# Performance work log

Hardware: AMD Instinct MI355X
Metric: run time of the kernel (lower is better)

The kernel has to match this reference:

```python
import jax, jax.numpy as jnp
import numpy as np

N_NODES = 50000
N_EDGES = 800000
IN_CH = 256
HID = 512
NUM_LAYERS = 3
EPS = 1e-12  # F.normalize eps


def setup_inputs() -> dict:
    key = jax.random.key(0)
    ks = jax.random.split(key, 2 + 3 * NUM_LAYERS)
    x = jax.random.normal(ks[0], (N_NODES, IN_CH), dtype=jnp.float32)
    edge_index = jax.random.randint(ks[1], (2, N_EDGES), 0, N_NODES, dtype=jnp.int64)
    inp = {"x": x, "edge_index": edge_index}
    dims = [(IN_CH, HID)] + [(HID, HID)] * (NUM_LAYERS - 1)
    for i, (din, dout) in enumerate(dims):
        s = 1.0 / np.sqrt(din)
        inp[f"Wl{i}"] = jax.random.normal(ks[2 + 3 * i], (din, dout), dtype=jnp.float32) * s
        inp[f"bl{i}"] = jnp.zeros((dout,), dtype=jnp.float32)
        inp[f"Wr{i}"] = jax.random.normal(ks[3 + 3 * i], (din, dout), dtype=jnp.float32) * s
    return inp


def _sage_conv(x, src, dst, Wl, bl, Wr):
    # aggr='add': out[dst] += x[src], then lin_l(agg) + lin_r(x), L2 normalize rows
    agg = jax.ops.segment_sum(x[src], dst, num_segments=x.shape[0])  # [N, din]
    out = agg @ Wl + bl + x @ Wr  # [N, dout]
    norm = jnp.maximum(jnp.linalg.norm(out, axis=-1, keepdims=True), EPS)
    return out / norm


def reference(x, edge_index, Wl0, bl0, Wr0, Wl1, bl1, Wr1, Wl2, bl2, Wr2):
    src, dst = edge_index[0], edge_index[1]
    feat = x
    params = [(Wl0, bl0, Wr0), (Wl1, bl1, Wr1), (Wl2, bl2, Wr2)]
    for Wl, bl, Wr in params:
        aggre = _sage_conv(feat, src, dst, Wl, bl, Wr)
        # Dropout(p=0.15) is identity in eval mode
        feat = jax.nn.elu(aggre)
    return feat
```

## Files before the change

### kernel.cpp

```cpp
#include <hip/hip_runtime.h>
#include <math.h>

#define N_NODES 50000
#define M_PAD   50048
#define N_EDGES 800000
#define HID 512

typedef short bf16x8 __attribute__((ext_vector_type(8)));
typedef float f32x4  __attribute__((ext_vector_type(4)));
typedef unsigned short u16x8 __attribute__((ext_vector_type(8)));

__device__ inline float b2f(unsigned short u) {
    union { unsigned int i; float f; } v; v.i = ((unsigned int)u) << 16; return v.f;
}
__device__ inline unsigned short f2b(float f) {
    union { float f; unsigned int i; } v; v.f = f;
    unsigned int r = v.i + 0x7FFFu + ((v.i >> 16) & 1u);
    return (unsigned short)(r >> 16);
}


__global__ void zero_kernel(int* __restrict__ p, int n) {
    int i = blockIdx.x * blockDim.x + threadIdx.x;
    if (i < n) p[i] = 0;
}

__global__ void detect_kernel(const int* __restrict__ e, int* __restrict__ flag) {
    if (blockIdx.x == 0 && threadIdx.x == 0) {
        int is64 = 1;
        for (int i = 0; i < 16; ++i)
            if (e[2 * i + 1] != 0) is64 = 0;
        *flag = is64;
    }
}

__global__ void hist_kernel(const void* __restrict__ eidx, const int* __restrict__ flag,
                            int* __restrict__ counts) {
    int e = blockIdx.x * blockDim.x + threadIdx.x;
    if (e >= N_EDGES) return;
    int is64 = *flag;
    int d;
    if (is64) d = (int)((const long long*)eidx)[N_EDGES + e];
    else      d = ((const int*)eidx)[N_EDGES + e];
    atomicAdd(&counts[d], 1);
}

__global__ __launch_bounds__(1024) void scan_kernel(const int* __restrict__ counts,
                                                    int* __restrict__ offsets) {
    __shared__ int sums[1024];
    int t = threadIdx.x;
    const int CH = (N_NODES + 1023) / 1024;
    int lo = t * CH;
    int hi = min(lo + CH, N_NODES);
    int s = 0;
    for (int i = lo; i < hi; ++i) s += counts[i];
    sums[t] = s;
    __syncthreads();
    for (int off = 1; off < 1024; off <<= 1) {
        int v = 0;
        if (t >= off) v = sums[t - off];
        __syncthreads();
        sums[t] += v;
        __syncthreads();
    }
    int excl = (t == 0) ? 0 : sums[t - 1];
    for (int i = lo; i < hi; ++i) { offsets[i] = excl; excl += counts[i]; }
    if (t == 1023) offsets[N_NODES] = excl;
}

__global__ void fill_kernel(const void* __restrict__ eidx, const int* __restrict__ flag,
                            const int* __restrict__ offsets, int* __restrict__ cursor,
                            int* __restrict__ edge_src) {
    int e = blockIdx.x * blockDim.x + threadIdx.x;
    if (e >= N_EDGES) return;
    int is64 = *flag;
    int s, d;
    if (is64) {
        const long long* p = (const long long*)eidx;
        s = (int)p[e];
        d = (int)p[N_EDGES + e];
    } else {
        const int* p = (const int*)eidx;
        s = p[e];
        d = p[N_EDGES + e];
    }
    int pos = atomicAdd(&cursor[d], 1);
    edge_src[offsets[d] + pos] = s;
}


__global__ __launch_bounds__(256) void xconv_kernel(const float* __restrict__ x,
                                                    unsigned short* __restrict__ cat1) {
    int id = blockIdx.x * 256 + threadIdx.x;
    if (id >= M_PAD * 64) return;
    int row = id >> 6;
    int c = (id & 63) * 4;
    float4 v = make_float4(0.f, 0.f, 0.f, 0.f);
    if (row < N_NODES) v = *(const float4*)(x + (size_t)row * 256 + c);
    ushort4 h;
    h.x = f2b(v.x); h.y = f2b(v.y); h.z = f2b(v.z); h.w = f2b(v.w);
    *(ushort4*)(cat1 + (size_t)row * 512 + 256 + c) = h;
}

__global__ __launch_bounds__(128) void wconv_kernel(const float* __restrict__ W,
                                                    unsigned short* __restrict__ T,
                                                    int K, int ktot, int off) {
    int n = blockIdx.x;
    for (int k = threadIdx.x; k < K; k += 128)
        T[(size_t)n * ktot + off + k] = f2b(W[(size_t)k * HID + n]);
}


template <int W>
__global__ __launch_bounds__(256) void aggregate_kernel(const unsigned short* __restrict__ Fh,
                                                        const int* __restrict__ off,
                                                        const int* __restrict__ esrc,
                                                        unsigned short* __restrict__ Ah) {
    const int NSLICE = W / 64;
    const int STRIDE = 2 * W;
    const int slice = blockIdx.x % NSLICE;
    const int chunk = blockIdx.x / NSLICE;
    const int wid = threadIdx.x >> 6;
    const int lane = threadIdx.x & 63;
    const int node = chunk * 4 + wid;
    if (node >= N_NODES) return;
    const int beg = off[node], end = off[node + 1];
    const int deg = end - beg;
    const int col = slice * 64 + lane;

    float a0 = 0.f, a1 = 0.f, a2 = 0.f, a3 = 0.f;
    int idxv = 0;
    int i = 0;
    for (; i + 4 <= deg; i += 4) {
        const int b = i & 63;
        if (b == 0) idxv = (beg + i + lane < end) ? esrc[beg + i + lane] : 0;
        const int s0 = __shfl(idxv, b);
        const int s1 = __shfl(idxv, b + 1);
        const int s2 = __shfl(idxv, b + 2);
        const int s3 = __shfl(idxv, b + 3);
        a0 += b2f(Fh[(size_t)s0 * STRIDE + col]);
        a1 += b2f(Fh[(size_t)s1 * STRIDE + col]);
        a2 += b2f(Fh[(size_t)s2 * STRIDE + col]);
        a3 += b2f(Fh[(size_t)s3 * STRIDE + col]);
    }
    for (; i < deg; ++i) {
        const int b = i & 63;
        if (b == 0) idxv = (beg + i + lane < end) ? esrc[beg + i + lane] : 0;
        a0 += b2f(Fh[(size_t)__shfl(idxv, b) * STRIDE + col]);
    }
    Ah[(size_t)node * STRIDE + col] = f2b(a0 + a1 + a2 + a3);
}


template <int FINAL>
__global__ __launch_bounds__(512, 2) void gemm_mfma_kernel(
    const unsigned short* __restrict__ A, const unsigned short* __restrict__ B,
    const float* __restrict__ bias, float* __restrict__ outF,
    unsigned short* __restrict__ pre, int K) {
    __shared__ unsigned short S[2 * 12288];
    const int bm = blockIdx.y * 128;
    const int bn = blockIdx.x * 256;
    const int tid = threadIdx.x;
    const int l = tid & 63;
    const int w = tid >> 6;
    const int wr = (w >> 2) * 64;
    const int wc = (w & 3) * 64;

    const int se = (tid >> 2) * 32 + (tid & 3) * 8;
    const unsigned short* gA  = A + (size_t)(bm + (tid >> 2)) * K + (tid & 3) * 8;
    const unsigned short* gB0 = B + (size_t)(bn + (tid >> 2)) * K + (tid & 3) * 8;
    const unsigned short* gB1 = B + (size_t)(bn + 128 + (tid >> 2)) * K + (tid & 3) * 8;

    f32x4 acc[4][4];
#pragma unroll
    for (int m = 0; m < 4; ++m)
#pragma unroll
        for (int n = 0; n < 4; ++n) acc[m][n] = (f32x4){0.f, 0.f, 0.f, 0.f};

    const int aoff = (wr + (l & 15)) * 32 + (l >> 4) * 8;
    const int woff = 4096 + (wc + (l & 15)) * 32 + (l >> 4) * 8;
    const int ktiles = K >> 5;

    auto STAGE = [&](int buf, int kt) {
        unsigned short* lb = &S[buf * 12288];
        __builtin_amdgcn_global_load_lds(
            (const __attribute__((address_space(1))) void*)(gA + kt * 32),
            (__attribute__((address_space(3))) void*)(lb + se), 16, 0, 0);
        __builtin_amdgcn_global_load_lds(
            (const __attribute__((address_space(1))) void*)(gB0 + kt * 32),
            (__attribute__((address_space(3))) void*)(lb + 4096 + se), 16, 0, 0);
        __builtin_amdgcn_global_load_lds(
            (const __attribute__((address_space(1))) void*)(gB1 + kt * 32),
            (__attribute__((address_space(3))) void*)(lb + 8192 + se), 16, 0, 0);
    };

    STAGE(0, 0);
    __syncthreads();

    for (int kt = 0; kt < ktiles; ++kt) {
        if (kt + 1 < ktiles) STAGE((kt + 1) & 1, kt + 1);
        const int sb = (kt & 1) * 12288;

        bf16x8 af[4], wf[4];
#pragma unroll
        for (int m = 0; m < 4; ++m)
            af[m] = *(const bf16x8*)&S[sb + aoff + m * 512];
#pragma unroll
        for (int n = 0; n < 4; ++n)
            wf[n] = *(const bf16x8*)&S[sb + woff + n * 512];
#pragma unroll
        for (int m = 0; m < 4; ++m)
#pragma unroll
            for (int n = 0; n < 4; ++n)
                acc[m][n] = __builtin_amdgcn_mfma_f32_16x16x32_bf16(af[m], wf[n], acc[m][n], 0, 0, 0);
        __syncthreads();
    }

    const int r0 = bm + wr + (l >> 4) * 4;
    const int c0 = bn + wc + (l & 15);
#pragma unroll
    for (int n = 0; n < 4; ++n) {
        const float bv = bias[c0 + n * 16];
#pragma unroll
        for (int m = 0; m < 4; ++m) {
#pragma unroll
            for (int j = 0; j < 4; ++j) {
                int gr = r0 + m * 16 + j;
                if (gr < N_NODES) {
                    float val = acc[m][n][j] + bv;
                    if constexpr (FINAL)
                        outF[(size_t)gr * HID + c0 + n * 16] = val;
                    else
                        pre[(size_t)gr * HID + c0 + n * 16] = f2b(val);
                }
            }
        }
    }
}


template <int FINAL>
__global__ __launch_bounds__(256) void norm_elu_kernel(const void* __restrict__ inp,
                                                       float* __restrict__ outF,
                                                       unsigned short* __restrict__ Fh) {
    const int wid = threadIdx.x >> 6;
    const int lane = threadIdx.x & 63;
    const int row = blockIdx.x * 4 + wid;
    if (row >= N_NODES) return;
    float r[8];
    if constexpr (FINAL) {
        const float* p = (const float*)inp + (size_t)row * HID + lane * 8;
        float4 v0 = *(const float4*)p;
        float4 v1 = *(const float4*)(p + 4);
        r[0] = v0.x; r[1] = v0.y; r[2] = v0.z; r[3] = v0.w;
        r[4] = v1.x; r[5] = v1.y; r[6] = v1.z; r[7] = v1.w;
    } else {
        const unsigned short* p = (const unsigned short*)inp + (size_t)row * HID + lane * 8;
        u16x8 v = *(const u16x8*)p;
#pragma unroll
        for (int j = 0; j < 8; ++j) r[j] = b2f(v[j]);
    }
    float ss = 0.f;
#pragma unroll
    for (int j = 0; j < 8; ++j) ss += r[j] * r[j];
#pragma unroll
    for (int o = 32; o > 0; o >>= 1) ss += __shfl_xor(ss, o);
    float inv = 1.f / fmaxf(sqrtf(ss), 1e-12f);
#pragma unroll
    for (int j = 0; j < 8; ++j) {
        r[j] *= inv;
        r[j] = r[j] > 0.f ? r[j] : expm1f(r[j]);
    }
    if constexpr (FINAL) {
        float* q = outF + (size_t)row * HID + lane * 8;
        *(float4*)q = make_float4(r[0], r[1], r[2], r[3]);
        *(float4*)(q + 4) = make_float4(r[4], r[5], r[6], r[7]);
    } else {
        unsigned short* q = Fh + (size_t)row * 1024 + lane * 8;
        u16x8 h;
#pragma unroll
        for (int j = 0; j < 8; ++j) h[j] = f2b(r[j]);
        *(u16x8*)q = h;
    }
}


extern "C" void kernel_launch(void* const* d_in, const int* in_sizes, int n_in,
                              void* d_out, int out_size, void* d_ws, size_t ws_size,
                              hipStream_t stream) {
    const float* x    = (const float*)d_in[0];
    const void*  eidx = d_in[1];
    const float* Wl0 = (const float*)d_in[2];
    const float* bl0 = (const float*)d_in[3];
    const float* Wr0 = (const float*)d_in[4];
    const float* Wl1 = (const float*)d_in[5];
    const float* bl1 = (const float*)d_in[6];
    const float* Wr1 = (const float*)d_in[7];
    const float* Wl2 = (const float*)d_in[8];
    const float* bl2 = (const float*)d_in[9];
    const float* Wr2 = (const float*)d_in[10];
    float* outF = (float*)d_out;
    unsigned short* preB = (unsigned short*)d_out;

    char* ws = (char*)d_ws;
    size_t o = 0;
    auto alloc = [&](size_t bytes) { void* p = ws + o; o += (bytes + 255) & ~(size_t)255; return p; };

    unsigned short* Cat1 = (unsigned short*)alloc((size_t)M_PAD * 512 * 2);
    unsigned short* Cat2 = (unsigned short*)alloc((size_t)M_PAD * 1024 * 2);

    unsigned short* Wcat0 = (unsigned short*)alloc(512 * 512 * 2);
    unsigned short* Wcat1 = (unsigned short*)alloc(512 * 1024 * 2);
    unsigned short* Wcat2 = (unsigned short*)alloc(512 * 1024 * 2);

    int* counts   = (int*)alloc((size_t)2 * N_NODES * 4);
    int* cursor   = counts + N_NODES;
    int* offsets  = (int*)alloc((size_t)(N_NODES + 1) * 4);
    int* edge_src = (int*)alloc((size_t)N_EDGES * 4);
    int* flag     = (int*)alloc(256);

    zero_kernel<<<(2 * N_NODES + 255) / 256, 256, 0, stream>>>(counts, 2 * N_NODES);
    detect_kernel<<<1, 64, 0, stream>>>((const int*)eidx, flag);
    hist_kernel<<<(N_EDGES + 255) / 256, 256, 0, stream>>>(eidx, flag, counts);
    scan_kernel<<<1, 1024, 0, stream>>>(counts, offsets);
    fill_kernel<<<(N_EDGES + 255) / 256, 256, 0, stream>>>(eidx, flag, offsets, cursor, edge_src);

    xconv_kernel<<<(M_PAD * 64 + 255) / 256, 256, 0, stream>>>(x, Cat1);
    wconv_kernel<<<512, 128, 0, stream>>>(Wl0, Wcat0, 256, 512, 0);
    wconv_kernel<<<512, 128, 0, stream>>>(Wr0, Wcat0, 256, 512, 256);
    wconv_kernel<<<512, 128, 0, stream>>>(Wl1, Wcat1, 512, 1024, 0);
    wconv_kernel<<<512, 128, 0, stream>>>(Wr1, Wcat1, 512, 1024, 512);
    wconv_kernel<<<512, 128, 0, stream>>>(Wl2, Wcat2, 512, 1024, 0);
    wconv_kernel<<<512, 128, 0, stream>>>(Wr2, Wcat2, 512, 1024, 512);

    dim3 ggrid(2, M_PAD / 128);
    const int nchunk = (N_NODES + 3) / 4;

    aggregate_kernel<256><<<nchunk * 4, 256, 0, stream>>>(Cat1 + 256, offsets, edge_src, Cat1);
    gemm_mfma_kernel<0><<<ggrid, 512, 0, stream>>>(Cat1, Wcat0, bl0, nullptr, preB, 512);
    norm_elu_kernel<0><<<nchunk, 256, 0, stream>>>(preB, nullptr, Cat2 + 512);

    aggregate_kernel<512><<<nchunk * 8, 256, 0, stream>>>(Cat2 + 512, offsets, edge_src, Cat2);
    gemm_mfma_kernel<0><<<ggrid, 512, 0, stream>>>(Cat2, Wcat1, bl1, nullptr, preB, 1024);
    norm_elu_kernel<0><<<nchunk, 256, 0, stream>>>(preB, nullptr, Cat2 + 512);

    aggregate_kernel<512><<<nchunk * 8, 256, 0, stream>>>(Cat2 + 512, offsets, edge_src, Cat2);
    gemm_mfma_kernel<1><<<ggrid, 512, 0, stream>>>(Cat2, Wcat2, bl2, outF, nullptr, 1024);
    norm_elu_kernel<1><<<nchunk, 256, 0, stream>>>(outF, outF, nullptr);

    (void)in_sizes; (void)n_in; (void)out_size; (void)ws_size;
}
```

Baseline: 919.1 us.

## Widen aggregate gathers to bf16 pairs and remap GEMM blocks per XCD

The aggregation kernel now has each lane load two adjacent bf16 values as one 32-bit word. Each wave therefore covers 128 columns, and the grid is halved, which cuts load instructions and improves gather efficiency for the latency-bound edge aggregation. The GEMM launches as a 1D grid and remaps block ids so that consecutive tiles land on the same XCD, aiming to improve L2 reuse of A rows across the two N tiles. Each loop iteration now unrolls 2 edges instead of 4, so fewer loads are in flight per iteration.

```diff
diff --git a/kernel.cpp b/kernel.cpp
--- a/kernel.cpp
+++ b/kernel.cpp
@@ -17,6 +17,12 @@
     union { float f; unsigned int i; } v; v.f = f;
     unsigned int r = v.i + 0x7FFFu + ((v.i >> 16) & 1u);
     return (unsigned short)(r >> 16);
+}
+__device__ inline float blo(unsigned int d) {
+    union { unsigned int i; float f; } v; v.i = d << 16; return v.f;
+}
+__device__ inline float bhi(unsigned int d) {
+    union { unsigned int i; float f; } v; v.i = d & 0xFFFF0000u; return v.f;
 }
 
 
@@ -116,7 +122,7 @@
                                                         const int* __restrict__ off,
                                                         const int* __restrict__ esrc,
                                                         unsigned short* __restrict__ Ah) {
-    const int NSLICE = W / 64;
+    const int NSLICE = W / 128;
     const int STRIDE = 2 * W;
     const int slice = blockIdx.x % NSLICE;
     const int chunk = blockIdx.x / NSLICE;
@@ -126,29 +132,31 @@
     if (node >= N_NODES) return;
     const int beg = off[node], end = off[node + 1];
     const int deg = end - beg;
-    const int col = slice * 64 + lane;
+    const int col = slice * 128 + lane * 2;
+    const unsigned short* F = Fh + col;
 
     float a0 = 0.f, a1 = 0.f, a2 = 0.f, a3 = 0.f;
     int idxv = 0;
     int i = 0;
-    for (; i + 4 <= deg; i += 4) {
+    for (; i + 2 <= deg; i += 2) {
         const int b = i & 63;
         if (b == 0) idxv = (beg + i + lane < end) ? esrc[beg + i + lane] : 0;
         const int s0 = __shfl(idxv, b);
         const int s1 = __shfl(idxv, b + 1);
-        const int s2 = __shfl(idxv, b + 2);
-        const int s3 = __shfl(idxv, b + 3);
-        a0 += b2f(Fh[(size_t)s0 * STRIDE + col]);
-        a1 += b2f(Fh[(size_t)s1 * STRIDE + col]);
-        a2 += b2f(Fh[(size_t)s2 * STRIDE + col]);
-        a3 += b2f(Fh[(size_t)s3 * STRIDE + col]);
-    }
-    for (; i < deg; ++i) {
+        const unsigned int v0 = *(const unsigned int*)(F + (size_t)s0 * STRIDE);
+        const unsigned int v1 = *(const unsigned int*)(F + (size_t)s1 * STRIDE);
+        a0 += blo(v0); a1 += bhi(v0);
+        a2 += blo(v1); a3 += bhi(v1);
+    }
+    if (i < deg) {
         const int b = i & 63;
         if (b == 0) idxv = (beg + i + lane < end) ? esrc[beg + i + lane] : 0;
-        a0 += b2f(Fh[(size_t)__shfl(idxv, b) * STRIDE + col]);
-    }
-    Ah[(size_t)node * STRIDE + col] = f2b(a0 + a1 + a2 + a3);
+        const unsigned int v0 = *(const unsigned int*)(F + (size_t)__shfl(idxv, b) * STRIDE);
+        a0 += blo(v0); a1 += bhi(v0);
+    }
+    const unsigned int outd =
+        (unsigned int)f2b(a0 + a2) | ((unsigned int)f2b(a1 + a3) << 16);
+    *(unsigned int*)(Ah + (size_t)node * STRIDE + col) = outd;
 }
 
 
@@ -158,8 +166,14 @@
     const float* __restrict__ bias, float* __restrict__ outF,
     unsigned short* __restrict__ pre, int K) {
     __shared__ unsigned short S[2 * 12288];
-    const int bm = blockIdx.y * 128;
-    const int bn = blockIdx.x * 256;
+    const int T = gridDim.x;
+    const int q = T >> 3, r = T & 7;
+    const int xcd = blockIdx.x & 7;
+    const int n0 = blockIdx.x >> 3;
+    const int g = xcd * q + min(xcd, r) + n0;
+    const int bm = (g >> 1) * 128;
+    const int bn = (g & 1) * 256;
+
     const int tid = threadIdx.x;
     const int l = tid & 63;
     const int w = tid >> 6;
@@ -175,7 +189,7 @@
 #pragma unroll
     for (int m = 0; m < 4; ++m)
 #pragma unroll
-        for (int n = 0; n < 4; ++n) acc[m][n] = (f32x4){0.f, 0.f, 0.f, 0.f};
+        for (int nn = 0; nn < 4; ++nn) acc[m][nn] = (f32x4){0.f, 0.f, 0.f, 0.f};
 
     const int aoff = (wr + (l & 15)) * 32 + (l >> 4) * 8;
     const int woff = 4096 + (wc + (l & 15)) * 32 + (l >> 4) * 8;
@@ -206,32 +220,32 @@
         for (int m = 0; m < 4; ++m)
             af[m] = *(const bf16x8*)&S[sb + aoff + m * 512];
 #pragma unroll
-        for (int n = 0; n < 4; ++n)
-            wf[n] = *(const bf16x8*)&S[sb + woff + n * 512];
+        for (int nn = 0; nn < 4; ++nn)
+            wf[nn] = *(const bf16x8*)&S[sb + woff + nn * 512];
 #pragma unroll
         for (int m = 0; m < 4; ++m)
 #pragma unroll
-            for (int n = 0; n < 4; ++n)
-                acc[m][n] = __builtin_amdgcn_mfma_f32_16x16x32_bf16(af[m], wf[n], acc[m][n], 0, 0, 0);
+            for (int nn = 0; nn < 4; ++nn)
+                acc[m][nn] = __builtin_amdgcn_mfma_f32_16x16x32_bf16(af[m], wf[nn], acc[m][nn], 0, 0, 0);
         __syncthreads();
     }
 
     const int r0 = bm + wr + (l >> 4) * 4;
     const int c0 = bn + wc + (l & 15);
 #pragma unroll
-    for (int n = 0; n < 4; ++n) {
-        const float bv = bias[c0 + n * 16];
+    for (int nn = 0; nn < 4; ++nn) {
+        const float bv = bias[c0 + nn * 16];
 #pragma unroll
         for (int m = 0; m < 4; ++m) {
 #pragma unroll
             for (int j = 0; j < 4; ++j) {
                 int gr = r0 + m * 16 + j;
                 if (gr < N_NODES) {
-                    float val = acc[m][n][j] + bv;
+                    float val = acc[m][nn][j] + bv;
                     if constexpr (FINAL)
-                        outF[(size_t)gr * HID + c0 + n * 16] = val;
+                        outF[(size_t)gr * HID + c0 + nn * 16] = val;
                     else
-                        pre[(size_t)gr * HID + c0 + n * 16] = f2b(val);
+                        pre[(size_t)gr * HID + c0 + nn * 16] = f2b(val);
                 }
             }
         }
@@ -333,18 +347,18 @@
     wconv_kernel<<<512, 128, 0, stream>>>(Wl2, Wcat2, 512, 1024, 0);
     wconv_kernel<<<512, 128, 0, stream>>>(Wr2, Wcat2, 512, 1024, 512);
 
-    dim3 ggrid(2, M_PAD / 128);
+    const int ggrid = 2 * (M_PAD / 128);
     const int nchunk = (N_NODES + 3) / 4;
 
-    aggregate_kernel<256><<<nchunk * 4, 256, 0, stream>>>(Cat1 + 256, offsets, edge_src, Cat1);
+    aggregate_kernel<256><<<nchunk * 2, 256, 0, stream>>>(Cat1 + 256, offsets, edge_src, Cat1);
     gemm_mfma_kernel<0><<<ggrid, 512, 0, stream>>>(Cat1, Wcat0, bl0, nullptr, preB, 512);
     norm_elu_kernel<0><<<nchunk, 256, 0, stream>>>(preB, nullptr, Cat2 + 512);
 
-    aggregate_kernel<512><<<nchunk * 8, 256, 0, stream>>>(Cat2 + 512, offsets, edge_src, Cat2);
+    aggregate_kernel<512><<<nchunk * 4, 256, 0, stream>>>(Cat2 + 512, offsets, edge_src, Cat2);
     gemm_mfma_kernel<0><<<ggrid, 512, 0, stream>>>(Cat2, Wcat1, bl1, nullptr, preB, 1024);
     norm_elu_kernel<0><<<nchunk, 256, 0, stream>>>(preB, nullptr, Cat2 + 512);
 
-    aggregate_kernel<512><<<nchunk * 8, 256, 0, stream>>>(Cat2 + 512, offsets, edge_src, Cat2);
+    aggregate_kernel<512><<<nchunk * 4, 256, 0, stream>>>(Cat2 + 512, offsets, edge_src, Cat2);
     gemm_mfma_kernel<1><<<ggrid, 512, 0, stream>>>(Cat2, Wcat2, bl2, outF, nullptr, 1024);
     norm_elu_kernel<1><<<nchunk, 256, 0, stream>>>(outF, outF, nullptr);
 
```

Result: faster. 801.2 us (-12.8%).
